# Performance work log

Hardware: AMD Instinct MI355X
Metric: run time of the kernel (lower is better)

Reference implementation:

```python
import jax, jax.numpy as jnp
import numpy as np

B, S, D = 2, 2048, 2048
H, KVH = 16, 4
HD = D // H  # 128


def _rope_angles(seq, head_dim):
    theta = 1.0 / (10000.0 ** (jnp.arange(0, head_dim, 2, dtype=jnp.float32) / head_dim))
    ang = jnp.arange(seq, dtype=jnp.float32)[:, None] * theta[None, :]  # [S, HD/2]
    return jnp.cos(ang), jnp.sin(ang)


def _apply_rotary(t, cos, sin):
    # t: [B, S, h, HD]; pairs are (even, odd) along last dim (view_as_complex semantics)
    tr = t[..., 0::2]
    ti = t[..., 1::2]
    c = cos[None, :, None, :]
    s = sin[None, :, None, :]
    out_r = tr * c - ti * s
    out_i = tr * s + ti * c
    return jnp.stack([out_r, out_i], axis=-1).reshape(t.shape)


def setup_inputs() -> dict:
    key = jax.random.key(0)
    ks = jax.random.split(key, 8)
    sd = 1.0 / np.sqrt(D)
    return {
        'x': jax.random.normal(ks[0], (B, S, D), dtype=jnp.float32),
        'wq': jax.random.normal(ks[1], (D, D), dtype=jnp.float32) * sd,
        'bq': jax.random.normal(ks[2], (D,), dtype=jnp.float32) * 0.01,
        'wk': jax.random.normal(ks[3], (D, KVH * HD), dtype=jnp.float32) * sd,
        'bk': jax.random.normal(ks[4], (KVH * HD,), dtype=jnp.float32) * 0.01,
        'wv': jax.random.normal(ks[5], (D, KVH * HD), dtype=jnp.float32) * sd,
        'bv': jax.random.normal(ks[6], (KVH * HD,), dtype=jnp.float32) * 0.01,
        'wo': jax.random.normal(ks[7], (D, D), dtype=jnp.float32) * sd,
    }


def reference(x, wq, bq, wk, bk, wv, bv, wo):
    b, s, d = x.shape
    q = (x @ wq + bq).reshape(b, s, H, HD)
    k = (x @ wk + bk).reshape(b, s, KVH, HD)
    v = (x @ wv + bv).reshape(b, s, KVH, HD)

    cos, sin = _rope_angles(s, HD)
    q = _apply_rotary(q, cos, sin)
    k = _apply_rotary(k, cos, sin)

    repeat = H // KVH
    k = jnp.repeat(k, repeat, axis=2)  # [B, S, H, HD]
    v = jnp.repeat(v, repeat, axis=2)

    scale = 1.0 / np.sqrt(HD)
    att_score = jnp.einsum('bqhd,bkhd->bqhk', q, k) * scale  # [B, S, H, S]
    att_weight = jax.nn.softmax(att_score, axis=-1)
    out = jnp.einsum('bqhk,bkhd->bqhd', att_weight, v)
    out = out.reshape(b, s, H * HD)
    return out @ wo
```

## Files before the change

### kernel.cpp

```cpp
#include <hip/hip_runtime.h>
#include <hip/hip_bf16.h>
#include <cstdint>

typedef __attribute__((ext_vector_type(4))) float f32x4;
typedef __attribute__((ext_vector_type(16))) float f32x16;
typedef __attribute__((ext_vector_type(8))) short bf16x8;
typedef __attribute__((ext_vector_type(4))) unsigned int u32x4;
typedef unsigned short u16;
typedef unsigned int u32;

__device__ __forceinline__ u16 f2b(float x) {
  __hip_bfloat16 h = __float2bfloat16(x);
  return *reinterpret_cast<u16*>(&h);
}

__device__ __forceinline__ u32 pk(float a, float b) {
  return ((u32)f2b(b) << 16) | (u32)f2b(a);
}

__device__ __forceinline__ void gload16(const void* g, void* l) {
  __builtin_amdgcn_global_load_lds((const __attribute__((address_space(1))) u32*)g,
                                   (__attribute__((address_space(3))) u32*)l, 16, 0, 0);
}

__device__ __forceinline__ float xmax32(float x) {
  return fmaxf(x, __shfl_xor(x, 32, 64));
}
__device__ __forceinline__ float xsum32(float x) {
  return x + __shfl_xor(x, 32, 64);
}


__global__ void cvt_f32_bf16(const float* __restrict__ in, u16* __restrict__ out, int n4) {
  int idx = (blockIdx.x * 256 + threadIdx.x);
  if (idx < n4) {
    const float4 v = *(const float4*)(in + (size_t)idx * 4);
    u16* o = out + (size_t)idx * 4;
    o[0] = f2b(v.x); o[1] = f2b(v.y); o[2] = f2b(v.z); o[3] = f2b(v.w);
  }
}

__global__ void w_transpose_cvt(const float* __restrict__ w0, const float* __restrict__ w1,
                                const float* __restrict__ w2, int b0, int b1,
                                int N0, int N1, int N2,
                                u16* __restrict__ out, int K) {
  __shared__ float tile[32][33];
  int k0 = blockIdx.x * 32, n0 = blockIdx.y * 32;
  const float* src; int srcN; int c0;
  if (n0 < b0)      { src = w0; srcN = N0; c0 = n0; }
  else if (n0 < b1) { src = w1; srcN = N1; c0 = n0 - b0; }
  else              { src = w2; srcN = N2; c0 = n0 - b1; }
  int tx = threadIdx.x & 31, ty = threadIdx.x >> 5;
#pragma unroll
  for (int j = 0; j < 32; j += 8)
    tile[ty + j][tx] = src[(size_t)(k0 + ty + j) * srcN + c0 + tx];
  __syncthreads();
#pragma unroll
  for (int j = 0; j < 32; j += 8)
    out[(size_t)(n0 + ty + j) * K + k0 + tx] = f2b(tile[tx][ty + j]);
}

__global__ void pack_bias(const float* __restrict__ bq, const float* __restrict__ bk,
                          const float* __restrict__ bv, float* __restrict__ out) {
  int i = blockIdx.x * 256 + threadIdx.x;
  if (i < 3072) out[i] = (i < 2048) ? bq[i] : ((i < 2560) ? bk[i - 2048] : bv[i - 2560]);
}

__global__ void v_transpose_cvt(const float* __restrict__ qkv, u16* __restrict__ vt) {
  __shared__ float tile[32][33];
  int s0 = blockIdx.x * 32;
  int d0 = blockIdx.y * 32;
  int z = blockIdx.z;
  int b = z >> 2, kvh = z & 3;
  int tx = threadIdx.x & 31, ty = threadIdx.x >> 5;
#pragma unroll
  for (int j = 0; j < 32; j += 8)
    tile[ty + j][tx] = qkv[((size_t)(b * 2048 + s0 + ty + j)) * 3072 + 2560 + kvh * 128 + d0 + tx];
  __syncthreads();
#pragma unroll
  for (int j = 0; j < 32; j += 8)
    vt[((size_t)z * 128 + d0 + ty + j) * 2048 + s0 + tx] = f2b(tile[tx][ty + j]);
}

__global__ void rope_cvt(const float* __restrict__ qkv, u16* __restrict__ out,
                         int lognh, int col0, float scale) {
  int idx = blockIdx.x * 256 + threadIdx.x;
  int i = idx & 63;
  int nh = 1 << lognh;
  int h = (idx >> 6) & (nh - 1);
  int bs = idx >> (6 + lognh);
  int s = bs & 2047;
  int b = bs >> 11;
  const float* src = qkv + (size_t)bs * 3072 + col0 + h * 128 + 2 * i;
  float tr = src[0], ti = src[1];
  float theta = expf(-(float)i * 0.14391156831212787f);
  float ang = (float)s * theta;
  float sv, cv;
  sincosf(ang, &sv, &cv);
  float orr = (tr * cv - ti * sv) * scale;
  float oii = (tr * sv + ti * cv) * scale;
  u16* dst = out + (((size_t)(b * nh + h) * 2048 + s) * 128 + 2 * i);
  dst[0] = f2b(orr);
  dst[1] = f2b(oii);
}

__global__ __launch_bounds__(256) void gemm_bt_bf16(
    const u16* __restrict__ A, const u16* __restrict__ Bt,
    const float* __restrict__ bias, float* __restrict__ C,
    int M, int N, int K) {
  __shared__ u16 As[128 * 32];
  __shared__ u16 Bs[128 * 32];
  const int tid = threadIdx.x;
  const int lane = tid & 63;
  const int w = tid >> 6;
  const int wr = w >> 1, wc = w & 1;
  const int m0 = blockIdx.y * 128;
  const int n0 = blockIdx.x * 128;

  f32x4 acc[4][4] = {};

  for (int k0 = 0; k0 < K; k0 += 32) {
#pragma unroll
    for (int it = 0; it < 2; ++it) {
      int c = tid + it * 256;
      int row = c >> 2;
      int off = (c & 3) * 8;
      gload16(A + (size_t)(m0 + row) * K + k0 + off, (u16*)As + w * 512 + it * 2048);
      gload16(Bt + (size_t)(n0 + row) * K + k0 + off, (u16*)Bs + w * 512 + it * 2048);
    }
    __syncthreads();
    const int col8 = (lane >> 4) * 8;
    bf16x8 a[4], bfr[4];
#pragma unroll
    for (int m = 0; m < 4; ++m)
      a[m] = *(const bf16x8*)&As[(wr * 64 + m * 16 + (lane & 15)) * 32 + col8];
#pragma unroll
    for (int n = 0; n < 4; ++n)
      bfr[n] = *(const bf16x8*)&Bs[(wc * 64 + n * 16 + (lane & 15)) * 32 + col8];
#pragma unroll
    for (int m = 0; m < 4; ++m)
#pragma unroll
      for (int n = 0; n < 4; ++n)
        acc[m][n] = __builtin_amdgcn_mfma_f32_16x16x32_bf16(a[m], bfr[n], acc[m][n], 0, 0, 0);
    __syncthreads();
  }

#pragma unroll
  for (int m = 0; m < 4; ++m) {
    int row = m0 + wr * 64 + m * 16 + ((lane >> 4) << 2);
#pragma unroll
    for (int n = 0; n < 4; ++n) {
      int col = n0 + wc * 64 + n * 16 + (lane & 15);
      float bvv = bias ? bias[col] : 0.f;
      float* cp = C + (size_t)row * N + col;
#pragma unroll
      for (int r = 0; r < 4; ++r) cp[(size_t)r * N] = acc[m][n][r] + bvv;
    }
  }
}

__global__ __launch_bounds__(128, 1) void flash_attn(
    const u16* __restrict__ Qr, const u16* __restrict__ Kr,
    const u16* __restrict__ Vt, u16* __restrict__ Att) {
  __shared__ u16 Ks[2][32 * 128];
  __shared__ u16 Vs[2][128 * 32];
  const int tid = threadIdx.x, lane = tid & 63, w = tid >> 6;
  const int lo = lane & 31, hi = lane >> 5;
  const int q0 = blockIdx.x * 128 + w * 64;
  const int h = blockIdx.y, b = blockIdx.z;
  const int kvh = h >> 2;

  const char* Khead = (const char*)(Kr + (size_t)(b * 4 + kvh) * 2048 * 128);
  const char* Vhead = (const char*)(Vt + (size_t)(b * 4 + kvh) * 128 * 2048);

  bf16x8 qf0[8], qf1[8];
  {
    const u16* qp = Qr + ((size_t)(b * 16 + h) * 2048 + q0 + lo) * 128 + hi * 8;
#pragma unroll
    for (int ds = 0; ds < 8; ++ds) qf0[ds] = *(const bf16x8*)(qp + ds * 16);
    qp += (size_t)32 * 128;
#pragma unroll
    for (int ds = 0; ds < 8; ++ds) qf1[ds] = *(const bf16x8*)(qp + ds * 16);
  }

#define STAGE(bufi, t)                                                        \
  {                                                                           \
    _Pragma("unroll")                                                         \
    for (int it = 0; it < 4; ++it) {                                          \
      int c = it * 128 + tid;                                                 \
      int krow = c >> 4;                                                      \
      int koff = krow * 256 + ((c & 15) << 4 ^ ((krow & 7) << 4));            \
      gload16(Khead + (size_t)(t) * 8192 + koff,                              \
              (u16*)Ks[bufi] + it * 1024 + w * 512);                          \
      int vrow = c >> 2;                                                      \
      int voff = vrow * 4096 + ((c & 3) << 4 ^ (((vrow >> 1) & 3) << 4));     \
      gload16(Vhead + (size_t)(t) * 64 + voff,                                \
              (u16*)Vs[bufi] + it * 1024 + w * 512);                          \
    }                                                                         \
  }

  f32x16 o0[4] = {}, o1[4] = {};
  float m_run0 = -3.0e38f, l_run0 = 0.f;
  float m_run1 = -3.0e38f, l_run1 = 0.f;
  const int swz = (lo & 7) << 4;
  const int vswz = ((lo >> 1) & 3) << 4;
  const int hi16 = hi * 16;

  STAGE(0, 0);
  __syncthreads();

  int buf = 0;
  for (int t = 0; t < 64; ++t) {
    int tn = (t < 63) ? t + 1 : 63;
    STAGE(buf ^ 1, tn);

    const char* Kb = (const char*)Ks[buf];
    const char* Vb = (const char*)Vs[buf];

    f32x16 s0 = {}, s1 = {};
    __builtin_amdgcn_s_setprio(1);
#pragma unroll
    for (int ds = 0; ds < 8; ++ds) {
      bf16x8 kf = *(const bf16x8*)(Kb + lo * 256 + ((ds * 32 + hi16) ^ swz));
      s0 = __builtin_amdgcn_mfma_f32_32x32x16_bf16(kf, qf0[ds], s0, 0, 0, 0);
      s1 = __builtin_amdgcn_mfma_f32_32x32x16_bf16(kf, qf1[ds], s1, 0, 0, 0);
    }
    __builtin_amdgcn_s_setprio(0);

    bf16x8 paA0, paB0, paA1, paB1;
#define SOFTPASS(S, MR, LR, OA, PA, PB)                                       \
    {                                                                         \
      float m01 = fmaxf(fmaxf(S[0], S[1]), fmaxf(S[2], S[3]));                \
      float m23 = fmaxf(fmaxf(S[4], S[5]), fmaxf(S[6], S[7]));                \
      float m45 = fmaxf(fmaxf(S[8], S[9]), fmaxf(S[10], S[11]));              \
      float m67 = fmaxf(fmaxf(S[12], S[13]), fmaxf(S[14], S[15]));            \
      float pmax = xmax32(fmaxf(fmaxf(m01, m23), fmaxf(m45, m67)));           \
      if (!__all(pmax - MR <= 8.0f)) {                                        \
        float mnew = fmaxf(MR, pmax);                                         \
        float rs = __expf(MR - mnew);                                         \
        MR = mnew;                                                            \
        LR *= rs;                                                             \
        _Pragma("unroll")                                                     \
        for (int r = 0; r < 16; ++r) {                                        \
          float rsr = __shfl(rs, (r & 3) + 8 * (r >> 2) + 4 * hi, 64);        \
          OA[0][r] *= rsr; OA[1][r] *= rsr; OA[2][r] *= rsr; OA[3][r] *= rsr; \
        }                                                                     \
      }                                                                       \
      float lsum = 0.f;                                                       \
      _Pragma("unroll")                                                       \
      for (int r = 0; r < 16; ++r) {                                          \
        float p = __expf(S[r] - MR); S[r] = p; lsum += p;                     \
      }                                                                       \
      LR += xsum32(lsum);                                                     \
      u32 a0 = pk(S[0], S[1]),   a1 = pk(S[2], S[3]);                         \
      u32 b0 = pk(S[4], S[5]),   b1 = pk(S[6], S[7]);                         \
      u32 t0 = hi ? a0 : b0, t1 = hi ? a1 : b1;                               \
      u32 r0 = __shfl_xor(t0, 32, 64), r1 = __shfl_xor(t1, 32, 64);           \
      u32x4 w0;                                                               \
      w0[0] = hi ? r0 : a0; w0[1] = hi ? r1 : a1;                             \
      w0[2] = hi ? b0 : r0; w0[3] = hi ? b1 : r1;                             \
      PA = __builtin_bit_cast(bf16x8, w0);                                    \
      u32 c0 = pk(S[8], S[9]),   c1 = pk(S[10], S[11]);                       \
      u32 d0 = pk(S[12], S[13]), d1 = pk(S[14], S[15]);                       \
      u32 t2 = hi ? c0 : d0, t3 = hi ? c1 : d1;                               \
      u32 r2 = __shfl_xor(t2, 32, 64), r3 = __shfl_xor(t3, 32, 64);           \
      u32x4 w1;                                                               \
      w1[0] = hi ? r2 : c0; w1[1] = hi ? r3 : c1;                             \
      w1[2] = hi ? d0 : r2; w1[3] = hi ? d1 : r3;                             \
      PB = __builtin_bit_cast(bf16x8, w1);                                    \
    }
    SOFTPASS(s0, m_run0, l_run0, o0, paA0, paB0)
    SOFTPASS(s1, m_run1, l_run1, o1, paA1, paB1)

    __builtin_amdgcn_s_setprio(1);
#pragma unroll
    for (int n = 0; n < 4; ++n) {
      const char* vrb = Vb + (n * 32 + lo) * 64;
      bf16x8 vb0 = *(const bf16x8*)(vrb + ((0  + hi16) ^ vswz));
      bf16x8 vb1 = *(const bf16x8*)(vrb + ((32 + hi16) ^ vswz));
      o0[n] = __builtin_amdgcn_mfma_f32_32x32x16_bf16(paA0, vb0, o0[n], 0, 0, 0);
      o0[n] = __builtin_amdgcn_mfma_f32_32x32x16_bf16(paB0, vb1, o0[n], 0, 0, 0);
      o1[n] = __builtin_amdgcn_mfma_f32_32x32x16_bf16(paA1, vb0, o1[n], 0, 0, 0);
      o1[n] = __builtin_amdgcn_mfma_f32_32x32x16_bf16(paB1, vb1, o1[n], 0, 0, 0);
    }
    __builtin_amdgcn_s_setprio(0);

    __syncthreads();
    buf ^= 1;
  }

  float inv0 = 1.0f / l_run0;
  float inv1 = 1.0f / l_run1;
  size_t rowbase = (size_t)(b * 2048 + q0);
#pragma unroll
  for (int r = 0; r < 16; ++r) {
    int rr = (r & 3) + 8 * (r >> 2) + 4 * hi;
    float iv0 = __shfl(inv0, rr, 64);
    float iv1 = __shfl(inv1, rr, 64);
    u16* op0 = Att + (rowbase + rr) * 2048 + h * 128 + lo;
    u16* op1 = Att + (rowbase + 32 + rr) * 2048 + h * 128 + lo;
    op0[0]  = f2b(o0[0][r] * iv0);
    op0[32] = f2b(o0[1][r] * iv0);
    op0[64] = f2b(o0[2][r] * iv0);
    op0[96] = f2b(o0[3][r] * iv0);
    op1[0]  = f2b(o1[0][r] * iv1);
    op1[32] = f2b(o1[1][r] * iv1);
    op1[64] = f2b(o1[2][r] * iv1);
    op1[96] = f2b(o1[3][r] * iv1);
  }
}


extern "C" void kernel_launch(void* const* d_in, const int* in_sizes, int n_in,
                              void* d_out, int out_size, void* d_ws, size_t ws_size,
                              hipStream_t stream) {
  const float* x  = (const float*)d_in[0];
  const float* wq = (const float*)d_in[1];
  const float* bq = (const float*)d_in[2];
  const float* wk = (const float*)d_in[3];
  const float* bk = (const float*)d_in[4];
  const float* wv = (const float*)d_in[5];
  const float* bv = (const float*)d_in[6];
  const float* wo = (const float*)d_in[7];
  float* out = (float*)d_out;
  char* ws = (char*)d_ws;

  u16*   x_bf   = (u16*)  (ws + 0);
  u16*   att    = (u16*)  (ws + 0);
  u16*   wqkv_t = (u16*)  (ws + 16777216);
  u16*   wo_t   = (u16*)  (ws + 29360128);
  float* biasq  = (float*)(ws + 37748736);
  float* qkv    = (float*)(ws + 37761024);
  u16*   q_r    = (u16*)  (ws + 88092672);
  u16*   k_r    = (u16*)  (ws + 104869888);
  u16*   v_t    = (u16*)  (ws + 109064192);

  cvt_f32_bf16<<<8192, 256, 0, stream>>>(x, x_bf, 2097152);
  w_transpose_cvt<<<dim3(64, 96), 256, 0, stream>>>(wq, wk, wv, 2048, 2560,
                                                    2048, 512, 512, wqkv_t, 2048);
  w_transpose_cvt<<<dim3(64, 64), 256, 0, stream>>>(wo, wo, wo, 2048, 2560,
                                                    2048, 2048, 2048, wo_t, 2048);
  pack_bias<<<12, 256, 0, stream>>>(bq, bk, bv, biasq);

  gemm_bt_bf16<<<dim3(24, 32), 256, 0, stream>>>(x_bf, wqkv_t, biasq, qkv, 4096, 3072, 2048);

  rope_cvt<<<16384, 256, 0, stream>>>(qkv, q_r, 4, 0, 0.08838834764831845f);
  rope_cvt<<<4096, 256, 0, stream>>>(qkv, k_r, 2, 2048, 1.0f);
  v_transpose_cvt<<<dim3(64, 4, 8), 256, 0, stream>>>(qkv, v_t);

  flash_attn<<<dim3(16, 16, 2), 128, 0, stream>>>(q_r, k_r, v_t, att);

  gemm_bt_bf16<<<dim3(16, 32), 256, 0, stream>>>(att, wo_t, nullptr, out, 4096, 2048, 2048);
}
```

Measured before the change: 303.1 us.

## Split attention KV range in two and merge partials in a combine kernel

The flash attention grid is doubled by splitting the key/value sequence into two halves. Each block writes unnormalized fp32 partial outputs plus running max and sum, and a new combine kernel merges them into bf16. The softmax switches to exp2 with log2(e) folded into the Q scale, the rescale threshold is raised, bf16 packing uses a paired conversion, and launch bounds now allow two blocks per CU. The aim is better CU occupancy, since the old 512-block grid underfilled the GPU. The cost is extra fp32 partial traffic and one more kernel launch.

Result: slower. 316.2 us (+4.3%).

```diff
diff --git a/kernel.cpp b/kernel.cpp
--- a/kernel.cpp
+++ b/kernel.cpp
@@ -15,7 +15,8 @@
 }
 
 __device__ __forceinline__ u32 pk(float a, float b) {
-  return ((u32)f2b(b) << 16) | (u32)f2b(a);
+  __hip_bfloat162 h2 = __float22bfloat162_rn(float2{a, b});
+  return *reinterpret_cast<u32*>(&h2);
 }
 
 __device__ __forceinline__ void gload16(const void* g, void* l) {
@@ -159,19 +160,23 @@
   }
 }
 
-__global__ __launch_bounds__(128, 1) void flash_attn(
+__global__ __launch_bounds__(128, 2) void flash_attn(
     const u16* __restrict__ Qr, const u16* __restrict__ Kr,
-    const u16* __restrict__ Vt, u16* __restrict__ Att) {
+    const u16* __restrict__ Vt, float* __restrict__ o_part,
+    float* __restrict__ mlbuf) {
   __shared__ u16 Ks[2][32 * 128];
   __shared__ u16 Vs[2][128 * 32];
   const int tid = threadIdx.x, lane = tid & 63, w = tid >> 6;
   const int lo = lane & 31, hi = lane >> 5;
   const int q0 = blockIdx.x * 128 + w * 64;
-  const int h = blockIdx.y, b = blockIdx.z;
+  const int h = blockIdx.y;
+  const int z = blockIdx.z;
+  const int b = z >> 1, split = z & 1;
   const int kvh = h >> 2;
-
-  const char* Khead = (const char*)(Kr + (size_t)(b * 4 + kvh) * 2048 * 128);
-  const char* Vhead = (const char*)(Vt + (size_t)(b * 4 + kvh) * 128 * 2048);
+  const int P = split * 32 + b * 16 + h;
+
+  const char* Khead = (const char*)(Kr + (size_t)(b * 4 + kvh) * 262144 + (size_t)split * 131072);
+  const char* Vhead = (const char*)(Vt + (size_t)(b * 4 + kvh) * 262144 + (size_t)split * 1024);
 
   bf16x8 qf0[8], qf1[8];
   {
@@ -210,8 +215,8 @@
   __syncthreads();
 
   int buf = 0;
-  for (int t = 0; t < 64; ++t) {
-    int tn = (t < 63) ? t + 1 : 63;
+  for (int t = 0; t < 32; ++t) {
+    int tn = (t < 31) ? t + 1 : 31;
     STAGE(buf ^ 1, tn);
 
     const char* Kb = (const char*)Ks[buf];
@@ -230,14 +235,17 @@
     bf16x8 paA0, paB0, paA1, paB1;
 #define SOFTPASS(S, MR, LR, OA, PA, PB)                                       \
     {                                                                         \
-      float m01 = fmaxf(fmaxf(S[0], S[1]), fmaxf(S[2], S[3]));                \
-      float m23 = fmaxf(fmaxf(S[4], S[5]), fmaxf(S[6], S[7]));                \
-      float m45 = fmaxf(fmaxf(S[8], S[9]), fmaxf(S[10], S[11]));              \
-      float m67 = fmaxf(fmaxf(S[12], S[13]), fmaxf(S[14], S[15]));            \
-      float pmax = xmax32(fmaxf(fmaxf(m01, m23), fmaxf(m45, m67)));           \
-      if (!__all(pmax - MR <= 8.0f)) {                                        \
+      float t0 = fmaxf(fmaxf(S[0], S[1]), S[2]);                              \
+      float t1 = fmaxf(fmaxf(S[3], S[4]), S[5]);                              \
+      float t2 = fmaxf(fmaxf(S[6], S[7]), S[8]);                              \
+      float t3 = fmaxf(fmaxf(S[9], S[10]), S[11]);                            \
+      float t4 = fmaxf(fmaxf(S[12], S[13]), S[14]);                           \
+      float u0m = fmaxf(fmaxf(t0, t1), t2);                                   \
+      float u1m = fmaxf(fmaxf(t3, t4), S[15]);                                \
+      float pmax = xmax32(fmaxf(u0m, u1m));                                   \
+      if (!__all(pmax - MR <= 11.0f)) {                                       \
         float mnew = fmaxf(MR, pmax);                                         \
-        float rs = __expf(MR - mnew);                                         \
+        float rs = exp2f(MR - mnew);                                          \
         MR = mnew;                                                            \
         LR *= rs;                                                             \
         _Pragma("unroll")                                                     \
@@ -249,21 +257,21 @@
       float lsum = 0.f;                                                       \
       _Pragma("unroll")                                                       \
       for (int r = 0; r < 16; ++r) {                                          \
-        float p = __expf(S[r] - MR); S[r] = p; lsum += p;                     \
+        float p = exp2f(S[r] - MR); S[r] = p; lsum += p;                      \
       }                                                                       \
       LR += xsum32(lsum);                                                     \
       u32 a0 = pk(S[0], S[1]),   a1 = pk(S[2], S[3]);                         \
       u32 b0 = pk(S[4], S[5]),   b1 = pk(S[6], S[7]);                         \
-      u32 t0 = hi ? a0 : b0, t1 = hi ? a1 : b1;                               \
-      u32 r0 = __shfl_xor(t0, 32, 64), r1 = __shfl_xor(t1, 32, 64);           \
+      u32 x0 = hi ? a0 : b0, x1 = hi ? a1 : b1;                               \
+      u32 r0 = __shfl_xor(x0, 32, 64), r1 = __shfl_xor(x1, 32, 64);           \
       u32x4 w0;                                                               \
       w0[0] = hi ? r0 : a0; w0[1] = hi ? r1 : a1;                             \
       w0[2] = hi ? b0 : r0; w0[3] = hi ? b1 : r1;                             \
       PA = __builtin_bit_cast(bf16x8, w0);                                    \
       u32 c0 = pk(S[8], S[9]),   c1 = pk(S[10], S[11]);                       \
       u32 d0 = pk(S[12], S[13]), d1 = pk(S[14], S[15]);                       \
-      u32 t2 = hi ? c0 : d0, t3 = hi ? c1 : d1;                               \
-      u32 r2 = __shfl_xor(t2, 32, 64), r3 = __shfl_xor(t3, 32, 64);           \
+      u32 x2 = hi ? c0 : d0, x3 = hi ? c1 : d1;                               \
+      u32 r2 = __shfl_xor(x2, 32, 64), r3 = __shfl_xor(x3, 32, 64);           \
       u32x4 w1;                                                               \
       w1[0] = hi ? r2 : c0; w1[1] = hi ? r3 : c1;                             \
       w1[2] = hi ? d0 : r2; w1[3] = hi ? d1 : r3;                             \
@@ -289,25 +297,43 @@
     buf ^= 1;
   }
 
-  float inv0 = 1.0f / l_run0;
-  float inv1 = 1.0f / l_run1;
-  size_t rowbase = (size_t)(b * 2048 + q0);
+  float* opp = o_part + ((size_t)P * 2048 + q0) * 128;
 #pragma unroll
   for (int r = 0; r < 16; ++r) {
     int rr = (r & 3) + 8 * (r >> 2) + 4 * hi;
-    float iv0 = __shfl(inv0, rr, 64);
-    float iv1 = __shfl(inv1, rr, 64);
-    u16* op0 = Att + (rowbase + rr) * 2048 + h * 128 + lo;
-    u16* op1 = Att + (rowbase + 32 + rr) * 2048 + h * 128 + lo;
-    op0[0]  = f2b(o0[0][r] * iv0);
-    op0[32] = f2b(o0[1][r] * iv0);
-    op0[64] = f2b(o0[2][r] * iv0);
-    op0[96] = f2b(o0[3][r] * iv0);
-    op1[0]  = f2b(o1[0][r] * iv1);
-    op1[32] = f2b(o1[1][r] * iv1);
-    op1[64] = f2b(o1[2][r] * iv1);
-    op1[96] = f2b(o1[3][r] * iv1);
-  }
+    float* p0 = opp + (size_t)rr * 128 + lo;
+    float* p1 = opp + (size_t)(32 + rr) * 128 + lo;
+    p0[0]  = o0[0][r]; p0[32] = o0[1][r]; p0[64] = o0[2][r]; p0[96] = o0[3][r];
+    p1[0]  = o1[0][r]; p1[32] = o1[1][r]; p1[64] = o1[2][r]; p1[96] = o1[3][r];
+  }
+  if (hi == 0) {
+    float2* mlp = (float2*)mlbuf;
+    mlp[P * 2048 + q0 + lo]      = float2{m_run0, l_run0};
+    mlp[P * 2048 + q0 + 32 + lo] = float2{m_run1, l_run1};
+  }
+}
+
+__global__ __launch_bounds__(256) void combine_att(
+    const float* __restrict__ o_part, const float* __restrict__ mlbuf,
+    u16* __restrict__ att) {
+  int tid = threadIdx.x;
+  int r = blockIdx.x * 8 + (tid >> 5);
+  int d4 = (tid & 31) * 4;
+  int bh = r >> 11, q = r & 2047;
+  const float2* mlp = (const float2*)mlbuf;
+  float2 ml0 = mlp[bh * 2048 + q];
+  float2 ml1 = mlp[(32 + bh) * 2048 + q];
+  float m = fmaxf(ml0.x, ml1.x);
+  float w0 = exp2f(ml0.x - m), w1 = exp2f(ml1.x - m);
+  float invl = 1.0f / (ml0.y * w0 + ml1.y * w1);
+  float4 a = *(const float4*)(o_part + ((size_t)bh * 2048 + q) * 128 + d4);
+  float4 c = *(const float4*)(o_part + ((size_t)(32 + bh) * 2048 + q) * 128 + d4);
+  ushort4 o;
+  o.x = f2b((a.x * w0 + c.x * w1) * invl);
+  o.y = f2b((a.y * w0 + c.y * w1) * invl);
+  o.z = f2b((a.z * w0 + c.z * w1) * invl);
+  o.w = f2b((a.w * w0 + c.w * w1) * invl);
+  *(ushort4*)(att + ((size_t)((bh >> 4) * 2048 + q)) * 2048 + (bh & 15) * 128 + d4) = o;
 }
 
 
@@ -326,14 +352,16 @@
   char* ws = (char*)d_ws;
 
   u16*   x_bf   = (u16*)  (ws + 0);
-  u16*   att    = (u16*)  (ws + 0);
   u16*   wqkv_t = (u16*)  (ws + 16777216);
-  u16*   wo_t   = (u16*)  (ws + 29360128);
-  float* biasq  = (float*)(ws + 37748736);
-  float* qkv    = (float*)(ws + 37761024);
-  u16*   q_r    = (u16*)  (ws + 88092672);
-  u16*   k_r    = (u16*)  (ws + 104869888);
-  u16*   v_t    = (u16*)  (ws + 109064192);
+  float* qkv    = (float*)(ws + 29360128);
+  float* o_part = (float*)(ws + 0);
+  float* mlbuf  = (float*)(ws + 67108864);
+  u16*   wo_t   = (u16*)  (ws + 79691776);
+  u16*   q_r    = (u16*)  (ws + 88080384);
+  u16*   att    = (u16*)  (ws + 88080384);
+  u16*   k_r    = (u16*)  (ws + 104857600);
+  u16*   v_t    = (u16*)  (ws + 109051904);
+  float* biasq  = (float*)(ws + 113246208);
 
   cvt_f32_bf16<<<8192, 256, 0, stream>>>(x, x_bf, 2097152);
   w_transpose_cvt<<<dim3(64, 96), 256, 0, stream>>>(wq, wk, wv, 2048, 2560,
@@ -344,11 +372,12 @@
 
   gemm_bt_bf16<<<dim3(24, 32), 256, 0, stream>>>(x_bf, wqkv_t, biasq, qkv, 4096, 3072, 2048);
 
-  rope_cvt<<<16384, 256, 0, stream>>>(qkv, q_r, 4, 0, 0.08838834764831845f);
+  rope_cvt<<<16384, 256, 0, stream>>>(qkv, q_r, 4, 0, 0.12751743871465216f);
   rope_cvt<<<4096, 256, 0, stream>>>(qkv, k_r, 2, 2048, 1.0f);
   v_transpose_cvt<<<dim3(64, 4, 8), 256, 0, stream>>>(qkv, v_t);
 
-  flash_attn<<<dim3(16, 16, 2), 128, 0, stream>>>(q_r, k_r, v_t, att);
+  flash_attn<<<dim3(16, 16, 4), 128, 0, stream>>>(q_r, k_r, v_t, o_part, mlbuf);
+  combine_att<<<8192, 256, 0, stream>>>(o_part, mlbuf, att);
 
   gemm_bt_bf16<<<dim3(16, 32), 256, 0, stream>>>(att, wo_t, nullptr, out, 4096, 2048, 2048);
 }
```
